# Kernel tuning notes

Hardware: AMD Instinct MI355X
Metric: run time of the kernel (lower is better)

Reference implementation:

```python
import jax, jax.numpy as jnp
import numpy as np

N, E, C = 50000, 800000, 128
NEG_SLOPE = 0.01

def leaky(v):
    return jnp.where(v >= 0, v, NEG_SLOPE * v)

def setup_inputs() -> dict:
    key = jax.random.key(0)
    ks = jax.random.split(key, 16)
    s = lambda *sh: 1.0 / np.sqrt(sh[0])
    return {
        "x": jax.random.normal(ks[0], (N, C), dtype=jnp.float32),
        "pos": jax.random.normal(ks[1], (N, 3), dtype=jnp.float32),
        "edge_index": jax.random.randint(ks[2], (2, E), 0, N, dtype=jnp.int64),
        # mlp_h: Linear(C,C) -> LeakyReLU -> Linear(C,3) -> Tanh
        "h_w1": jax.random.uniform(ks[3], (C, C), jnp.float32, -s(C), s(C)),
        "h_b1": jax.random.uniform(ks[4], (C,), jnp.float32, -s(C), s(C)),
        "h_w2": jax.random.uniform(ks[5], (C, 3), jnp.float32, -s(C), s(C)),
        "h_b2": jax.random.uniform(ks[6], (3,), jnp.float32, -s(C), s(C)),
        # mlp_f: Linear(C+3, C) -> LeakyReLU
        "f_w": jax.random.uniform(ks[7], (C + 3, C), jnp.float32, -s(C + 3), s(C + 3)),
        "f_b": jax.random.uniform(ks[8], (C,), jnp.float32, -s(C + 3), s(C + 3)),
        # mlp_g: Linear(C,C) -> LeakyReLU -> Linear(C,C)
        "g_w1": jax.random.uniform(ks[9], (C, C), jnp.float32, -s(C), s(C)),
        "g_b1": jax.random.uniform(ks[10], (C,), jnp.float32, -s(C), s(C)),
        "g_w2": jax.random.uniform(ks[11], (C, C), jnp.float32, -s(C), s(C)),
        "g_b2": jax.random.uniform(ks[12], (C,), jnp.float32, -s(C), s(C)),
    }

def reference(x, pos, edge_index, h_w1, h_b1, h_w2, h_b2, f_w, f_b,
              g_w1, g_b1, g_w2, g_b2):
    src = edge_index[0]  # j (source)
    dst = edge_index[1]  # i (target)
    # delta_i = mlp_h(x_i): [N, 3]
    delta = jnp.tanh(leaky(x @ h_w1 + h_b1) @ h_w2 + h_b2)
    # edge message: mlp_f(cat([pos_j - pos_i + delta_i, x_j]))  -> [E, C]
    rel = pos[src] - pos[dst] + delta[dst]            # [E, 3]
    msg_in = jnp.concatenate([rel, x[src]], axis=-1)  # [E, C+3]
    e = leaky(msg_in @ f_w + f_b)                     # [E, C]
    # sum-aggregate messages at target nodes
    aggr = jax.ops.segment_sum(e, dst, num_segments=N)  # [N, C]
    # out = mlp_g(aggr) + x
    out = leaky(aggr @ g_w1 + g_b1) @ g_w2 + g_b2 + x
    return out
```

## Files before the change

kernel.cpp:

```cpp
#include <hip/hip_runtime.h>
#include <hip/hip_bf16.h>
#include <math.h>


typedef __attribute__((ext_vector_type(8))) short bf16x8;
typedef __attribute__((ext_vector_type(4))) float f32x4;

#define LEAKY(v) ((v) >= 0.0f ? (v) : 0.01f * (v))

#define KMAX 512
#define S3_BATCH 4096
#define HB 256
#define AGG_CAP 16384

static __device__ __forceinline__ unsigned short f2bf(float f) {
    unsigned u = __float_as_uint(f);
    u = (u + 0x7fffu + ((u >> 16) & 1u)) >> 16;
    return (unsigned short)u;
}

union ABu { unsigned short u[8]; bf16x8 v; };

static __device__ __forceinline__ bf16x8 cvt8(const float* __restrict__ p) {
    ABu r;
    const float4 v0 = *(const float4*)p;
    const float4 v1 = *(const float4*)(p + 4);
    r.u[0] = f2bf(v0.x); r.u[1] = f2bf(v0.y); r.u[2] = f2bf(v0.z); r.u[3] = f2bf(v0.w);
    r.u[4] = f2bf(v1.x); r.u[5] = f2bf(v1.y); r.u[6] = f2bf(v1.z); r.u[7] = f2bf(v1.w);
    return r.v;
}

static __device__ __forceinline__ bf16x8 zero_ab() {
    ABu r;
    #pragma unroll
    for (int i = 0; i < 8; ++i) r.u[i] = 0;
    return r.v;
}

static __device__ __forceinline__ void proc8(
    const uint4 v, const float* __restrict__ qd, float* __restrict__ acc)
{
    const float f0 = __uint_as_float((v.x & 0xffffu) << 16);
    const float f1 = __uint_as_float(v.x & 0xffff0000u);
    const float f2 = __uint_as_float((v.y & 0xffffu) << 16);
    const float f3 = __uint_as_float(v.y & 0xffff0000u);
    const float f4 = __uint_as_float((v.z & 0xffffu) << 16);
    const float f5 = __uint_as_float(v.z & 0xffff0000u);
    const float f6 = __uint_as_float((v.w & 0xffffu) << 16);
    const float f7 = __uint_as_float(v.w & 0xffff0000u);
    const float z0 = f0 + qd[0], z1 = f1 + qd[1];
    const float z2 = f2 + qd[2], z3 = f3 + qd[3];
    const float z4 = f4 + qd[4], z5 = f5 + qd[5];
    const float z6 = f6 + qd[6], z7 = f7 + qd[7];
    acc[0] += fmaxf(z0, 0.01f * z0);
    acc[1] += fmaxf(z1, 0.01f * z1);
    acc[2] += fmaxf(z2, 0.01f * z2);
    acc[3] += fmaxf(z3, 0.01f * z3);
    acc[4] += fmaxf(z4, 0.01f * z4);
    acc[5] += fmaxf(z5, 0.01f * z5);
    acc[6] += fmaxf(z6, 0.01f * z6);
    acc[7] += fmaxf(z7, 0.01f * z7);
}

static __device__ __forceinline__ int wave_incl_scan(int v) {
    const int lane = threadIdx.x & 63;
    #pragma unroll
    for (int d = 1; d < 64; d <<= 1) {
        const int t = __shfl_up(v, d);
        if (lane >= d) v += t;
    }
    return v;
}

static __device__ __forceinline__ void stage_weight(
    const unsigned short* __restrict__ src, unsigned short (*dst)[136], int tid)
{
    #pragma unroll
    for (int it = 0; it < 8; ++it) {
        const int c   = it * 256 + tid;
        const int row = c >> 4;
        const int col = (c & 15) * 8;
        *(uint4*)&dst[row][col] = *(const uint4*)(src + row * 128 + col);
    }
}

__global__ __launch_bounds__(128) void prep_weights(
    const float* __restrict__ h_w1, const float* __restrict__ f_w,
    const float* __restrict__ g_w1, const float* __restrict__ g_w2,
    unsigned short* __restrict__ Wht, unsigned short* __restrict__ Wft,
    unsigned short* __restrict__ G1t, unsigned short* __restrict__ G2t,
    int* __restrict__ bincnt, int* __restrict__ done)
{
    const int j = blockIdx.x;
    const int k = threadIdx.x;
    if (j == 0) {
        for (int i = k; i < KMAX; i += 128) bincnt[i] = 0;
        if (k == 0) *done = 0;
    }
    Wht[j * 128 + k] = f2bf(h_w1[(size_t)k * 128 + j]);
    Wft[j * 128 + k] = f2bf(f_w[(size_t)(3 + k) * 128 + j]);
    G1t[j * 128 + k] = f2bf(g_w1[(size_t)k * 128 + j]);
    G2t[j * 128 + k] = f2bf(g_w2[(size_t)k * 128 + j]);
}

__global__ __launch_bounds__(256) void fused_pre(
    const float* __restrict__ x, const float* __restrict__ pos,
    const unsigned short* __restrict__ Wht, const float* __restrict__ h_b1,
    const float* __restrict__ h_w2, const float* __restrict__ h_b2,
    const unsigned short* __restrict__ Wft, const float* __restrict__ f_b,
    const float* __restrict__ fw3,
    float* __restrict__ deltap, unsigned short* __restrict__ Zb,
    const int* __restrict__ ei, int* __restrict__ bincnt,
    int* __restrict__ binstart, int* __restrict__ cursors,
    int* __restrict__ done, int E, int K, int N)
{
    __shared__ __align__(16) unsigned char smem[34816 + 4096];
    __shared__ int lastflag;

    const int tid = threadIdx.x;

    if (blockIdx.x < HB) {
        int* h = (int*)smem;
        int* s = (int*)(smem + 2048);
        for (int k = tid; k < K; k += 256) h[k] = 0;
        __syncthreads();
        if ((E & 3) == 0) {
            const int E4 = E >> 2;
            const uint4* d4 = (const uint4*)(ei + (size_t)E);
            for (int i = blockIdx.x * 256 + tid; i < E4; i += HB * 256) {
                const uint4 v = d4[i];
                atomicAdd(&h[v.x >> 7], 1);
                atomicAdd(&h[v.y >> 7], 1);
                atomicAdd(&h[v.z >> 7], 1);
                atomicAdd(&h[v.w >> 7], 1);
            }
        } else {
            for (int e = blockIdx.x * 256 + tid; e < E; e += HB * 256)
                atomicAdd(&h[ei[(size_t)E + e] >> 7], 1);
        }
        __syncthreads();
        for (int k = tid; k < K; k += 256) {
            const int v = h[k];
            if (v) atomicAdd(&bincnt[k], v);
        }
        __threadfence();
        __syncthreads();
        if (tid == 0) lastflag = (atomicAdd(done, 1) == HB - 1) ? 1 : 0;
        __syncthreads();
        if (!lastflag) return;

        const int i0 = tid * 2;
        const int c0 = (i0 < K)     ? atomicAdd(&bincnt[i0], 0)     : 0;
        const int c1 = (i0 + 1 < K) ? atomicAdd(&bincnt[i0 + 1], 0) : 0;
        s[tid] = c0 + c1;
        __syncthreads();
        for (int d = 1; d < 256; d <<= 1) {
            const int t = (tid >= d) ? s[tid - d] : 0;
            __syncthreads();
            s[tid] += t;
            __syncthreads();
        }
        const int ex = s[tid] - (c0 + c1);
        if (i0 < K)     { binstart[i0]     = ex;      cursors[i0]     = ex; }
        if (i0 + 1 < K) { binstart[i0 + 1] = ex + c0; cursors[i0 + 1] = ex + c0; }
        if (tid == 0) binstart[K] = E;
        return;
    }

    unsigned short (*Ws)[136] = (unsigned short (*)[136])smem;
    float (*cb)[8] = (float (*)[8])(smem + 34816);

    const int lane = tid & 63;
    const int wave = tid >> 6;
    const int quad = lane >> 4;
    const int l16  = lane & 15;
    const int row0 = (blockIdx.x - HB) * 64 + wave * 16;

    if (tid < 128) {
        cb[tid][0] = h_b1[tid];
        cb[tid][1] = f_b[tid];
        cb[tid][2] = h_w2[tid * 3 + 0];
        cb[tid][3] = h_w2[tid * 3 + 1];
        cb[tid][4] = h_w2[tid * 3 + 2];
        cb[tid][5] = fw3[tid];
        cb[tid][6] = fw3[128 + tid];
        cb[tid][7] = fw3[256 + tid];
    }
    stage_weight(Wht, Ws, tid);

    bf16x8 a[4];
    {
        const int row = row0 + l16;
        if (row < N) {
            const float* xp = x + (size_t)row * 128 + quad * 8;
            #pragma unroll
            for (int kc = 0; kc < 4; ++kc) a[kc] = cvt8(xp + kc * 32);
        } else {
            #pragma unroll
            for (int kc = 0; kc < 4; ++kc) a[kc] = zero_ab();
        }
    }

    float px[4], py[4], pz[4];
    #pragma unroll
    for (int reg = 0; reg < 4; ++reg) {
        const int grow = row0 + quad * 4 + reg;
        const int gr = (grow < N) ? grow : 0;
        px[reg] = pos[(size_t)gr * 3 + 0];
        py[reg] = pos[(size_t)gr * 3 + 1];
        pz[reg] = pos[(size_t)gr * 3 + 2];
    }
    __syncthreads();

    f32x4 acch[8];
    #pragma unroll
    for (int nt = 0; nt < 8; ++nt) acch[nt] = (f32x4){0.f, 0.f, 0.f, 0.f};
    #pragma unroll
    for (int nt = 0; nt < 8; ++nt) {
        const unsigned short* wp = &Ws[nt * 16 + l16][quad * 8];
        #pragma unroll
        for (int kc = 0; kc < 4; ++kc) {
            const bf16x8 b = *(const bf16x8*)(wp + kc * 32);
            acch[nt] = __builtin_amdgcn_mfma_f32_16x16x32_bf16(a[kc], b, acch[nt], 0, 0, 0);
        }
    }

    __syncthreads();
    stage_weight(Wft, Ws, tid);
    __syncthreads();

    f32x4 accf[8];
    #pragma unroll
    for (int nt = 0; nt < 8; ++nt) accf[nt] = (f32x4){0.f, 0.f, 0.f, 0.f};
    #pragma unroll
    for (int nt = 0; nt < 8; ++nt) {
        const unsigned short* wp = &Ws[nt * 16 + l16][quad * 8];
        #pragma unroll
        for (int kc = 0; kc < 4; ++kc) {
            const bf16x8 b = *(const bf16x8*)(wp + kc * 32);
            accf[nt] = __builtin_amdgcn_mfma_f32_16x16x32_bf16(a[kc], b, accf[nt], 0, 0, 0);
        }
    }

    float p[4][3];
    #pragma unroll
    for (int r = 0; r < 4; ++r) { p[r][0] = 0.f; p[r][1] = 0.f; p[r][2] = 0.f; }

    #pragma unroll
    for (int nt = 0; nt < 8; ++nt) {
        const int col = nt * 16 + l16;
        const float b1  = cb[col][0];
        const float fb  = cb[col][1];
        const float w20 = cb[col][2];
        const float w21 = cb[col][3];
        const float w22 = cb[col][4];
        const float wxc = cb[col][5];
        const float wyc = cb[col][6];
        const float wzc = cb[col][7];
        #pragma unroll
        for (int reg = 0; reg < 4; ++reg) {
            const int grow = row0 + quad * 4 + reg;
            float h = acch[nt][reg] + b1;
            h = LEAKY(h);
            p[reg][0] += h * w20;
            p[reg][1] += h * w21;
            p[reg][2] += h * w22;
            if (grow < N) {
                const float z = accf[nt][reg] + fb
                              + px[reg] * wxc + py[reg] * wyc + pz[reg] * wzc;
                Zb[(size_t)grow * 128 + col] = f2bf(z);
            }
        }
    }

    #pragma unroll
    for (int reg = 0; reg < 4; ++reg)
        #pragma unroll
        for (int c = 0; c < 3; ++c) {
            float v = p[reg][c];
            v += __shfl_down(v, 8);
            v += __shfl_down(v, 4);
            v += __shfl_down(v, 2);
            v += __shfl_down(v, 1);
            p[reg][c] = v;
        }

    if (l16 == 0) {
        #pragma unroll
        for (int reg = 0; reg < 4; ++reg) {
            const int grow = row0 + quad * 4 + reg;
            if (grow < N) {
                deltap[(size_t)grow * 3 + 0] = tanhf(p[reg][0] + h_b2[0]) - px[reg];
                deltap[(size_t)grow * 3 + 1] = tanhf(p[reg][1] + h_b2[1]) - py[reg];
                deltap[(size_t)grow * 3 + 2] = tanhf(p[reg][2] + h_b2[2]) - pz[reg];
            }
        }
    }
}

__global__ __launch_bounds__(512) void binsort(
    const int* __restrict__ ei, int* __restrict__ cursors,
    unsigned int* __restrict__ binned, int E, int K)
{
    __shared__ int h[KMAX];
    __shared__ int hE[KMAX];
    __shared__ int cur[KMAX];
    __shared__ int gbase[KMAX];
    __shared__ int wsum[8];
    __shared__ unsigned int stage[S3_BATCH];

    const int tid = threadIdx.x;
    const int e0  = blockIdx.x * S3_BATCH;
    const int m   = min(S3_BATCH, E - e0);
    const bool vec = (m == S3_BATCH) && ((E & 3) == 0);

    for (int k = tid; k < K; k += 512) h[k] = 0;
    __syncthreads();

    unsigned int dsts[8];
    if (vec) {
        const uint4* dv = (const uint4*)(ei + (size_t)E + e0);
        const uint4 a0 = dv[tid];
        const uint4 a1 = dv[tid + 512];
        dsts[0] = a0.x; dsts[1] = a0.y; dsts[2] = a0.z; dsts[3] = a0.w;
        dsts[4] = a1.x; dsts[5] = a1.y; dsts[6] = a1.z; dsts[7] = a1.w;
        #pragma unroll
        for (int j = 0; j < 8; ++j) atomicAdd(&h[dsts[j] >> 7], 1);
    } else {
        #pragma unroll
        for (int j = 0; j < 8; ++j) {
            const int i = (j < 4) ? (4 * tid + j) : (S3_BATCH / 2 + 4 * tid + j - 4);
            dsts[j] = 0;
            if (i < m) {
                dsts[j] = (unsigned int)ei[(size_t)E + e0 + i];
                atomicAdd(&h[dsts[j] >> 7], 1);
            }
        }
    }
    __syncthreads();

    {
        const int c = (tid < K) ? h[tid] : 0;
        int sc = wave_incl_scan(c);
        if ((tid & 63) == 63) wsum[tid >> 6] = sc;
        __syncthreads();
        if (tid < 64) {
            int w = (tid < 8) ? wsum[tid] : 0;
            #pragma unroll
            for (int d = 1; d < 8; d <<= 1) {
                const int t = __shfl_up(w, d);
                if (tid >= d) w += t;
            }
            if (tid < 8) wsum[tid] = w;
        }
        __syncthreads();
        if (tid >= 64) sc += wsum[(tid >> 6) - 1];
        if (tid < K) {
            const int ex = sc - c;
            hE[tid]  = ex;
            cur[tid] = ex;
            gbase[tid] = c ? atomicAdd(&cursors[tid], c) : 0;
        }
    }
    __syncthreads();

    if (vec) {
        const uint4* sv = (const uint4*)(ei + (size_t)e0);
        const uint4 b0 = sv[tid];
        const uint4 b1 = sv[tid + 512];
        unsigned int srcs[8];
        srcs[0] = b0.x; srcs[1] = b0.y; srcs[2] = b0.z; srcs[3] = b0.w;
        srcs[4] = b1.x; srcs[5] = b1.y; srcs[6] = b1.z; srcs[7] = b1.w;
        #pragma unroll
        for (int j = 0; j < 8; ++j) {
            const int p = atomicAdd(&cur[dsts[j] >> 7], 1);
            stage[p] = srcs[j] | (dsts[j] << 16);
        }
    } else {
        #pragma unroll
        for (int j = 0; j < 8; ++j) {
            const int i = (j < 4) ? (4 * tid + j) : (S3_BATCH / 2 + 4 * tid + j - 4);
            if (i < m) {
                const unsigned int src = (unsigned int)ei[(size_t)e0 + i];
                const int p = atomicAdd(&cur[dsts[j] >> 7], 1);
                stage[p] = src | (dsts[j] << 16);
            }
        }
    }
    __syncthreads();

    #pragma unroll
    for (int j = 0; j < S3_BATCH / 512; ++j) {
        const int i = j * 512 + tid;
        if (i < m) {
            const unsigned int r = stage[i];
            const int k = r >> 23;
            binned[(size_t)gbase[k] + (i - hE[k])] = r & 0x007FFFFFu;
        }
    }
}

__global__ __launch_bounds__(512) void bin_csr_aggregate(
    const unsigned int* __restrict__ binned, const int* __restrict__ binstart,
    const float* __restrict__ deltap,
    const unsigned short* __restrict__ Zb,
    const float* __restrict__ fw3,
    unsigned short* __restrict__ srcs_g,
    unsigned short* __restrict__ Ab,
    int N)
{
    __shared__ int h[64];
    __shared__ int s[64];
    __shared__ int cur[64];
    __shared__ unsigned short sl[AGG_CAP];

    const int tid  = threadIdx.x;
    const int bin  = blockIdx.x >> 1;
    const int half = blockIdx.x & 1;
    const int s0   = binstart[bin];
    const int s1   = binstart[bin + 1];
    const int len  = s1 - s0;

    if (tid < 64) h[tid] = 0;
    __syncthreads();

    for (int i = tid; i < len; i += 512) {
        const int dl16 = binned[(size_t)s0 + i] >> 16;
        if ((dl16 >> 6) == half) atomicAdd(&h[dl16 & 63], 1);
    }
    __syncthreads();

    if (tid < 64) {
        const int hv = h[tid];
        const int sc = wave_incl_scan(hv);
        s[tid]   = sc;
        cur[tid] = sc - hv;
    }
    __syncthreads();

    const int own   = s[63];
    const bool fits = (own <= AGG_CAP);
    const int gb    = half ? (s1 - own) : s0;

    for (int i = tid; i < len; i += 512) {
        const unsigned int r = binned[(size_t)s0 + i];
        const int dl16 = r >> 16;
        if ((dl16 >> 6) == half) {
            const int p = atomicAdd(&cur[dl16 & 63], 1);
            if (fits) sl[p] = (unsigned short)(r & 0xffffu);
            else      srcs_g[(size_t)gb + p] = (unsigned short)(r & 0xffffu);
        }
    }
    __threadfence_block();
    __syncthreads();

    const int lane    = tid & 63;
    const int wv      = tid >> 6;
    const int quarter = lane >> 4;
    const int cl      = (lane & 15) * 8;
    const int d0      = bin * 128 + half * 64;

    for (int dl = wv; dl < 64; dl += 8) {
        const int d = d0 + dl;
        if (d >= N) continue;

        const int len_d = h[dl];
        const int start = s[dl] - h[dl];

        const float q0 = deltap[(size_t)d * 3 + 0];
        const float q1 = deltap[(size_t)d * 3 + 1];
        const float q2 = deltap[(size_t)d * 3 + 2];

        float qd[8];
        #pragma unroll
        for (int j = 0; j < 8; ++j)
            qd[j] = q0 * fw3[cl + j] + q1 * fw3[128 + cl + j] + q2 * fw3[256 + cl + j];

        float acc[8] = {0.f, 0.f, 0.f, 0.f, 0.f, 0.f, 0.f, 0.f};

        for (int chunk = 0; chunk < len_d; chunk += 64) {
            const int m = min(64, len_d - chunk);
            int idx = 0;
            if (lane < m)
                idx = fits ? (int)sl[start + chunk + lane]
                           : (int)srcs_g[(size_t)gb + start + chunk + lane];

            int t = 0;
            #pragma unroll 4
            for (; t + 4 <= m; t += 4) {
                const int sidx = __shfl(idx, t + quarter);
                const uint4 y = *(const uint4*)(Zb + (size_t)sidx * 128 + cl);
                proc8(y, qd, acc);
            }
            if (t < m) {
                const int e = t + quarter;
                const int sidx = __shfl(idx, e);
                if (e < m) {
                    const uint4 y = *(const uint4*)(Zb + (size_t)sidx * 128 + cl);
                    proc8(y, qd, acc);
                }
            }
        }

        #pragma unroll
        for (int j = 0; j < 8; ++j) {
            acc[j] += __shfl_xor(acc[j], 16);
            acc[j] += __shfl_xor(acc[j], 32);
        }
        if (quarter == 0) {
            ABu o;
            #pragma unroll
            for (int j = 0; j < 8; ++j) o.u[j] = f2bf(acc[j]);
            *(bf16x8*)(Ab + (size_t)d * 128 + cl) = o.v;
        }
    }
}

__global__ __launch_bounds__(256) void gemm_g(
    const unsigned short* __restrict__ Ab,
    const unsigned short* __restrict__ G1t, const float* __restrict__ g_b1,
    const unsigned short* __restrict__ G2t, const float* __restrict__ g_b2,
    const float* __restrict__ x,
    float* __restrict__ out, int N)
{
    __shared__ unsigned short Ws[128][136];
    __shared__ unsigned short Ts[64][136];

    const int tid  = threadIdx.x;
    const int lane = tid & 63;
    const int wave = tid >> 6;
    const int quad = lane >> 4;
    const int l16  = lane & 15;
    const int row0 = blockIdx.x * 64 + wave * 16;

    stage_weight(G1t, Ws, tid);

    bf16x8 a[4];
    {
        const int row = row0 + l16;
        if (row < N) {
            const unsigned short* ap = Ab + (size_t)row * 128 + quad * 8;
            #pragma unroll
            for (int kc = 0; kc < 4; ++kc) a[kc] = *(const bf16x8*)(ap + kc * 32);
        } else {
            #pragma unroll
            for (int kc = 0; kc < 4; ++kc) a[kc] = zero_ab();
        }
    }
    __syncthreads();

    f32x4 acc[8];
    #pragma unroll
    for (int nt = 0; nt < 8; ++nt) acc[nt] = (f32x4){0.f, 0.f, 0.f, 0.f};
    #pragma unroll
    for (int nt = 0; nt < 8; ++nt) {
        const unsigned short* wp = &Ws[nt * 16 + l16][quad * 8];
        #pragma unroll
        for (int kc = 0; kc < 4; ++kc) {
            const bf16x8 b = *(const bf16x8*)(wp + kc * 32);
            acc[nt] = __builtin_amdgcn_mfma_f32_16x16x32_bf16(a[kc], b, acc[nt], 0, 0, 0);
        }
    }

    #pragma unroll
    for (int nt = 0; nt < 8; ++nt) {
        const int col = nt * 16 + l16;
        const float b1 = g_b1[col];
        #pragma unroll
        for (int reg = 0; reg < 4; ++reg) {
            float t = acc[nt][reg] + b1;
            t = LEAKY(t);
            Ts[wave * 16 + quad * 4 + reg][col] = f2bf(t);
        }
    }
    __syncthreads();
    stage_weight(G2t, Ws, tid);
    __syncthreads();

    bf16x8 a2[4];
    {
        const unsigned short* tp = &Ts[wave * 16 + l16][quad * 8];
        #pragma unroll
        for (int kc = 0; kc < 4; ++kc) a2[kc] = *(const bf16x8*)(tp + kc * 32);
    }

    f32x4 acc2[8];
    #pragma unroll
    for (int nt = 0; nt < 8; ++nt) acc2[nt] = (f32x4){0.f, 0.f, 0.f, 0.f};
    #pragma unroll
    for (int nt = 0; nt < 8; ++nt) {
        const unsigned short* wp = &Ws[nt * 16 + l16][quad * 8];
        #pragma unroll
        for (int kc = 0; kc < 4; ++kc) {
            const bf16x8 b = *(const bf16x8*)(wp + kc * 32);
            acc2[nt] = __builtin_amdgcn_mfma_f32_16x16x32_bf16(a2[kc], b, acc2[nt], 0, 0, 0);
        }
    }

    #pragma unroll
    for (int nt = 0; nt < 8; ++nt) {
        const int col = nt * 16 + l16;
        const float b2 = g_b2[col];
        #pragma unroll
        for (int reg = 0; reg < 4; ++reg) {
            const int grow = row0 + quad * 4 + reg;
            if (grow < N)
                out[(size_t)grow * 128 + col] =
                    acc2[nt][reg] + b2 + x[(size_t)grow * 128 + col];
        }
    }
}

extern "C" void kernel_launch(void* const* d_in, const int* in_sizes, int n_in,
                              void* d_out, int out_size, void* d_ws, size_t ws_size,
                              hipStream_t stream) {
    const float* x    = (const float*)d_in[0];
    const float* pos  = (const float*)d_in[1];
    const int*   ei   = (const int*)d_in[2];
    const float* h_w1 = (const float*)d_in[3];
    const float* h_b1 = (const float*)d_in[4];
    const float* h_w2 = (const float*)d_in[5];
    const float* h_b2 = (const float*)d_in[6];
    const float* f_w  = (const float*)d_in[7];
    const float* f_b  = (const float*)d_in[8];
    const float* g_w1 = (const float*)d_in[9];
    const float* g_b1 = (const float*)d_in[10];
    const float* g_w2 = (const float*)d_in[11];
    const float* g_b2 = (const float*)d_in[12];
    float* out = (float*)d_out;

    const int N = in_sizes[0] / 128;
    const int E = in_sizes[2] / 2;
    const int K = (N + 127) >> 7;

    float* deltap         = (float*)d_ws;
    unsigned short* Zb    = (unsigned short*)(deltap + (size_t)N * 3);
    int* bincnt           = (int*)(Zb + (size_t)N * 128);
    int* binstart         = bincnt + KMAX;
    int* cursors          = binstart + (KMAX + 1);
    int* done             = cursors + KMAX;
    unsigned int* binned  = (unsigned int*)(done + 1);
    unsigned short* srcs  = (unsigned short*)(binned + E);
    unsigned short* Wht   = srcs + (((size_t)E + 1) & ~(size_t)1);
    unsigned short* Wft   = Wht + 128 * 128;
    unsigned short* G1t   = Wft + 128 * 128;
    unsigned short* G2t   = G1t + 128 * 128;
    unsigned short* Ab    = G2t + 128 * 128;

    const int tile_blocks = (N + 63) / 64;
    const int sort_blocks = (E + S3_BATCH - 1) / S3_BATCH;

    prep_weights<<<128, 128, 0, stream>>>(h_w1, f_w, g_w1, g_w2, Wht, Wft, G1t, G2t,
                                          bincnt, done);

    fused_pre<<<HB + tile_blocks, 256, 0, stream>>>(
        x, pos, Wht, h_b1, h_w2, h_b2, Wft, f_b, f_w,
        deltap, Zb, ei, bincnt, binstart, cursors, done, E, K, N);

    binsort<<<sort_blocks, 512, 0, stream>>>(ei, cursors, binned, E, K);

    bin_csr_aggregate<<<K * 2, 512, 0, stream>>>(binned, binstart, deltap, Zb, f_w,
                                                 srcs, Ab, N);

    gemm_g<<<tile_blocks, 256, 0, stream>>>(Ab, G1t, g_b1, G2t, g_b2, x, out, N);
}
```

Before: 216.4 us.

## Split aggregation blocks by channel half instead of destination half

The aggregation kernel now gives each block a whole 128-node bin but only 64 of the 128 channels, with block indices interleaved so the two channel-half blocks of a bin run close together. Each wave handles 8 edges per step with 8 lanes per row. The aim is to shrink each gathered row segment to 128 bytes, so the two halves of the same bin can share the source rows in L2, and to balance work across blocks by channel rather than by uneven destination counts. In exchange, every block rebuilds the full bin histogram and CSR (duplicated work), the reduction needs an extra shuffle step, and the global fallback buffer doubles to 2E entries.

Result: slower. 234.9 us (+8.6%).

```diff
diff --git a/kernel.cpp b/kernel.cpp
--- a/kernel.cpp
+++ b/kernel.cpp
@@ -400,67 +400,64 @@
     }
 }
 
-__global__ __launch_bounds__(512) void bin_csr_aggregate(
+__global__ __launch_bounds__(512) void bin_agg_chalf(
     const unsigned int* __restrict__ binned, const int* __restrict__ binstart,
     const float* __restrict__ deltap,
     const unsigned short* __restrict__ Zb,
     const float* __restrict__ fw3,
     unsigned short* __restrict__ srcs_g,
     unsigned short* __restrict__ Ab,
-    int N)
+    int E, int K, int N)
 {
-    __shared__ int h[64];
-    __shared__ int s[64];
-    __shared__ int cur[64];
+    __shared__ int h[128];
+    __shared__ int s[128];
+    __shared__ int cur[128];
     __shared__ unsigned short sl[AGG_CAP];
 
-    const int tid  = threadIdx.x;
-    const int bin  = blockIdx.x >> 1;
-    const int half = blockIdx.x & 1;
-    const int s0   = binstart[bin];
-    const int s1   = binstart[bin + 1];
-    const int len  = s1 - s0;
-
-    if (tid < 64) h[tid] = 0;
-    __syncthreads();
-
-    for (int i = tid; i < len; i += 512) {
-        const int dl16 = binned[(size_t)s0 + i] >> 16;
-        if ((dl16 >> 6) == half) atomicAdd(&h[dl16 & 63], 1);
-    }
-    __syncthreads();
-
-    if (tid < 64) {
-        const int hv = h[tid];
-        const int sc = wave_incl_scan(hv);
-        s[tid]   = sc;
-        cur[tid] = sc - hv;
-    }
-    __syncthreads();
-
-    const int own   = s[63];
-    const bool fits = (own <= AGG_CAP);
-    const int gb    = half ? (s1 - own) : s0;
+    const int tid   = threadIdx.x;
+    const int g     = blockIdx.x & 7;
+    const int chalf = g >> 2;
+    const int bin   = (blockIdx.x >> 3) * 4 + (g & 3);
+    if (bin >= K) return;
+
+    const int s0  = binstart[bin];
+    const int s1  = binstart[bin + 1];
+    const int len = s1 - s0;
+
+    if (tid < 128) h[tid] = 0;
+    __syncthreads();
+
+    for (int i = tid; i < len; i += 512)
+        atomicAdd(&h[binned[(size_t)s0 + i] >> 16], 1);
+    __syncthreads();
+
+    if (tid < 128) s[tid] = wave_incl_scan(h[tid]);
+    __syncthreads();
+    if (tid >= 64 && tid < 128) s[tid] += s[63];
+    __syncthreads();
+    if (tid < 128) cur[tid] = s[tid] - h[tid];
+    __syncthreads();
+
+    const bool fits = (len <= AGG_CAP);
+    const size_t gbase = (size_t)chalf * E + s0;
 
     for (int i = tid; i < len; i += 512) {
         const unsigned int r = binned[(size_t)s0 + i];
-        const int dl16 = r >> 16;
-        if ((dl16 >> 6) == half) {
-            const int p = atomicAdd(&cur[dl16 & 63], 1);
-            if (fits) sl[p] = (unsigned short)(r & 0xffffu);
-            else      srcs_g[(size_t)gb + p] = (unsigned short)(r & 0xffffu);
-        }
+        const int p = atomicAdd(&cur[r >> 16], 1);
+        if (fits) sl[p] = (unsigned short)(r & 0xffffu);
+        else      srcs_g[gbase + p] = (unsigned short)(r & 0xffffu);
     }
     __threadfence_block();
     __syncthreads();
 
-    const int lane    = tid & 63;
-    const int wv      = tid >> 6;
-    const int quarter = lane >> 4;
-    const int cl      = (lane & 15) * 8;
-    const int d0      = bin * 128 + half * 64;
-
-    for (int dl = wv; dl < 64; dl += 8) {
+    const int lane = tid & 63;
+    const int wv   = tid >> 6;
+    const int oct  = lane >> 3;
+    const int co   = (lane & 7) * 8;
+    const int chb  = chalf * 64 + co;
+    const int d0   = bin * 128;
+
+    for (int dl = wv; dl < 128; dl += 8) {
         const int d = d0 + dl;
         if (d >= N) continue;
 
@@ -474,7 +471,7 @@
         float qd[8];
         #pragma unroll
         for (int j = 0; j < 8; ++j)
-            qd[j] = q0 * fw3[cl + j] + q1 * fw3[128 + cl + j] + q2 * fw3[256 + cl + j];
+            qd[j] = q0 * fw3[chb + j] + q1 * fw3[128 + chb + j] + q2 * fw3[256 + chb + j];
 
         float acc[8] = {0.f, 0.f, 0.f, 0.f, 0.f, 0.f, 0.f, 0.f};
 
@@ -483,20 +480,20 @@
             int idx = 0;
             if (lane < m)
                 idx = fits ? (int)sl[start + chunk + lane]
-                           : (int)srcs_g[(size_t)gb + start + chunk + lane];
+                           : (int)srcs_g[gbase + start + chunk + lane];
 
             int t = 0;
             #pragma unroll 4
-            for (; t + 4 <= m; t += 4) {
-                const int sidx = __shfl(idx, t + quarter);
-                const uint4 y = *(const uint4*)(Zb + (size_t)sidx * 128 + cl);
+            for (; t + 8 <= m; t += 8) {
+                const int sidx = __shfl(idx, t + oct);
+                const uint4 y = *(const uint4*)(Zb + (size_t)sidx * 128 + chb);
                 proc8(y, qd, acc);
             }
             if (t < m) {
-                const int e = t + quarter;
+                const int e = t + oct;
                 const int sidx = __shfl(idx, e);
                 if (e < m) {
-                    const uint4 y = *(const uint4*)(Zb + (size_t)sidx * 128 + cl);
+                    const uint4 y = *(const uint4*)(Zb + (size_t)sidx * 128 + chb);
                     proc8(y, qd, acc);
                 }
             }
@@ -504,14 +501,15 @@
 
         #pragma unroll
         for (int j = 0; j < 8; ++j) {
+            acc[j] += __shfl_xor(acc[j], 8);
             acc[j] += __shfl_xor(acc[j], 16);
             acc[j] += __shfl_xor(acc[j], 32);
         }
-        if (quarter == 0) {
+        if (oct == 0) {
             ABu o;
             #pragma unroll
             for (int j = 0; j < 8; ++j) o.u[j] = f2bf(acc[j]);
-            *(bf16x8*)(Ab + (size_t)d * 128 + cl) = o.v;
+            *(bf16x8*)(Ab + (size_t)d * 128 + chb) = o.v;
         }
     }
 }
@@ -641,7 +639,7 @@
     int* done             = cursors + KMAX;
     unsigned int* binned  = (unsigned int*)(done + 1);
     unsigned short* srcs  = (unsigned short*)(binned + E);
-    unsigned short* Wht   = srcs + (((size_t)E + 1) & ~(size_t)1);
+    unsigned short* Wht   = srcs + ((((size_t)E * 2) + 1) & ~(size_t)1);
     unsigned short* Wft   = Wht + 128 * 128;
     unsigned short* G1t   = Wft + 128 * 128;
     unsigned short* G2t   = G1t + 128 * 128;
@@ -649,6 +647,7 @@
 
     const int tile_blocks = (N + 63) / 64;
     const int sort_blocks = (E + S3_BATCH - 1) / S3_BATCH;
+    const int agg_blocks  = ((K + 3) >> 2) * 8;
 
     prep_weights<<<128, 128, 0, stream>>>(h_w1, f_w, g_w1, g_w2, Wht, Wft, G1t, G2t,
                                           bincnt, done);
@@ -659,8 +658,8 @@
 
     binsort<<<sort_blocks, 512, 0, stream>>>(ei, cursors, binned, E, K);
 
-    bin_csr_aggregate<<<K * 2, 512, 0, stream>>>(binned, binstart, deltap, Zb, f_w,
-                                                 srcs, Ab, N);
+    bin_agg_chalf<<<agg_blocks, 512, 0, stream>>>(binned, binstart, deltap, Zb, f_w,
+                                                  srcs, Ab, E, K, N);
 
     gemm_g<<<tile_blocks, 256, 0, stream>>>(Ab, G1t, g_b1, G2t, g_b2, x, out, N);
 }
```
